# Optimization experiments

Measured on AMD Instinct MI355X. Metric: run time of the kernel, lower is better.

The kernel has to match this reference:

```python
import jax, jax.numpy as jnp
import numpy as np

B, V, S, F, K = 8, 2048, 4, 64, 8
MAX_DIST = np.float32(np.finfo(np.float32).max)


def setup_inputs() -> dict:
    key = jax.random.key(0)
    k1, k2 = jax.random.split(key)
    coordinates = jax.random.normal(k1, (B, V, S), dtype=jnp.float32)
    features = jax.random.normal(k2, (B, V, F), dtype=jnp.float32)
    # per-event number of active vertices (float, compared against the raw mask)
    active_vertices = jnp.full((B, 1), 0.75 * V, dtype=jnp.float32)
    return {"coordinates": coordinates, "features": features,
            "active_vertices": active_vertices}


def reference(coordinates, features, active_vertices):
    # squared euclidean distance matrix: |x_i - x_j|^2 = -2 x_i.x_j + |x_i|^2 + |x_j|^2
    sub = -2.0 * jnp.einsum('bvs,bws->bvw', coordinates, coordinates)
    dot = jnp.sum(coordinates * coordinates, axis=2)  # [B, V]
    dist = jnp.abs(sub + dot[:, :, None] + dot[:, None, :])  # [B, V, V]

    # raw mask: max(row_idx, col_idx); vertex pair valid iff both < n_active
    r = jnp.arange(V)
    raw_mask = jnp.maximum(r[None, :], r[:, None]).astype(jnp.float32)  # [V, V]
    mask = raw_mask[None, :, :] < active_vertices[:, :, None]  # [B, V, V]
    dist = jnp.where(mask, dist, MAX_DIST)

    # top-k smallest distances (self at rank 0 is dropped)
    neg_ranked, idx = jax.lax.top_k(-dist, K)  # [B, V, K]
    neighbour_idx = idx[:, :, 1:]              # [B, V, K-1]
    neighbour_distances = -neg_ranked[:, :, 1:]

    # gather neighbour features per batch: [B, V, K-1, F]
    batch_idx = jnp.arange(B)[:, None, None]
    neighbour_features = features[batch_idx, neighbour_idx]
    return neighbour_distances, neighbour_features
```

## Files before the change

kernel.cpp:

```cpp
#include <hip/hip_runtime.h>
#include <cstdint>
#include <cfloat>
#include <cstddef>

#define BB 8
#define VV 2048
#define SS 4
#define FF 64
#define KK 8

#define BF16_SAFE_MAX 3.3e38f

typedef unsigned long long u64;
typedef unsigned int u32;

static __forceinline__ __device__ double mk_key(float sd_clamped, u32 w) {
    return __longlong_as_double(
        __double_as_longlong((double)sd_clamped) | (long long)w);
}
static __forceinline__ __device__ u32 key_idx(double k) {
    return (u32)((u64)__double_as_longlong(k) & (u64)(VV - 1));
}
static __forceinline__ __device__ double shfl_xor_f64(double x, int m) {
    const u64 b = (u64)__double_as_longlong(x);
    int lo = __shfl_xor((int)(u32)b, m, 64);
    int hi = __shfl_xor((int)(u32)(b >> 32), m, 64);
    return __longlong_as_double((long long)(((u64)(u32)hi << 32) | (u32)lo));
}

#define CED(A, x, y) { double lo_ = fmin(A[x], A[y]);                          \
                       double hi_ = fmax(A[x], A[y]);                          \
                       A[x] = lo_; A[y] = hi_; }

#define SORT8D(K, O)                                                           \
    CED(K,O+0,O+1) CED(K,O+2,O+3) CED(K,O+4,O+5) CED(K,O+6,O+7)                \
    CED(K,O+0,O+2) CED(K,O+1,O+3) CED(K,O+4,O+6) CED(K,O+5,O+7)                \
    CED(K,O+1,O+2) CED(K,O+5,O+6)                                              \
    CED(K,O+0,O+4) CED(K,O+1,O+5) CED(K,O+2,O+6) CED(K,O+3,O+7)                \
    CED(K,O+2,O+4) CED(K,O+3,O+5)                                              \
    CED(K,O+1,O+2) CED(K,O+3,O+4) CED(K,O+5,O+6)

#define CLEAN8D(t)                                                             \
    CED(t,0,4) CED(t,1,5) CED(t,2,6) CED(t,3,7)                                \
    CED(t,0,2) CED(t,1,3) CED(t,4,6) CED(t,5,7)                                \
    CED(t,0,1) CED(t,2,3) CED(t,4,5) CED(t,6,7)

#define MERGE8D(T, S) {                                                        \
    double t[KK];                                                              \
    t[0] = fmin(T[0], S[7]);  t[1] = fmin(T[1], S[6]);                         \
    t[2] = fmin(T[2], S[5]);  t[3] = fmin(T[3], S[4]);                         \
    t[4] = fmin(T[4], S[3]);  t[5] = fmin(T[5], S[2]);                         \
    t[6] = fmin(T[6], S[1]);  t[7] = fmin(T[7], S[0]);                         \
    CLEAN8D(t)                                                                 \
    T[0]=t[0]; T[1]=t[1]; T[2]=t[2]; T[3]=t[3];                                \
    T[4]=t[4]; T[5]=t[5]; T[6]=t[6]; T[7]=t[7]; }

#define BATCH_S8(M, S8)                                                        \
    {                                                                          \
        double bk[16];                                                         \
        _Pragma("unroll")                                                      \
        for (int k = 0; k < 16; ++k) {                                         \
            const int w  = (((M) << 4) + k) * 32 + l;           \
            const int wi = w & (VV / 2 - 1);                  \
            const float4 cw = sc[wi];                                          \
            const float  nw = sn[wi];                                          \
            float q0 = cv.x*cw.x, q1 = cv.y*cw.y,                              \
                  q2 = cv.z*cw.z, q3 = cv.w*cw.w;                              \
            float dotp = ((q0 + q1) + q2) + q3;         \
            float sd = dotp + nvp;                                             \
            sd = sd + nw;                                                      \
            const float sda = fminf(fabsf(sd), FLT_MAX);                       \
            bk[k] = mk_key(sda, (u32)w);                                       \
        }                                                                      \
        SORT8D(bk, 0)                                                          \
        SORT8D(bk, 8)                                                          \
        S8[0] = fmin(bk[0], bk[15]); S8[1] = fmin(bk[1], bk[14]);              \
        S8[2] = fmin(bk[2], bk[13]); S8[3] = fmin(bk[3], bk[12]);              \
        S8[4] = fmin(bk[4], bk[11]); S8[5] = fmin(bk[5], bk[10]);              \
        S8[6] = fmin(bk[6], bk[9]);  S8[7] = fmin(bk[7], bk[8]);               \
        CLEAN8D(S8)                                                            \
    }

__global__ __launch_bounds__(256, 6)
void knn_topk_kernel(const float* __restrict__ coords,
                     const float* __restrict__ feats,
                     const float* __restrict__ active,
                     float* __restrict__ out_dist,
                     float* __restrict__ out_feat)
{
#pragma clang fp contract(off)
    __shared__ float4 sc[VV / 2];
    __shared__ float  sn[VV / 2];

    const int b   = blockIdx.y;
    const int tid = threadIdx.x;
    const int l   = tid & 31;
    const int j   = tid >> 5;
    const int v   = blockIdx.x + (j << 8);

    const float A = active[b];
    int Ai = (int)ceilf(A);
    Ai = Ai < 0 ? 0 : (Ai > VV ? VV : Ai);

    const size_t row = (size_t)b * VV + v;
    const float4* cg = reinterpret_cast<const float4*>(coords + (size_t)b * VV * SS);

    const bool rowActive = ((float)v < A);
    const bool heavy = (__ballot(rowActive) != 0ULL);

    const float4 cv = cg[v];
    float qp0 = cv.x*cv.x, qp1 = cv.y*cv.y, qp2 = cv.z*cv.z, qp3 = cv.w*cv.w;
    const float nv  = ((qp0 + qp1) + qp2) + qp3;
    const float nvp = rowActive ? nv : FLT_MAX;

    double top[KK];

    int ntiles = (Ai + 31) >> 5;
    if (ntiles < 16) ntiles = 16;
    const int nb = (ntiles + 15) >> 4;

#define STAGE(P, LIM)                                                          \
    for (int i = tid; i < (LIM); i += 256) {                                   \
        const float4 c = cg[i + ((P) << 10)];                                  \
        float p0 = c.x*c.x, p1 = c.y*c.y, p2 = c.z*c.z, p3 = c.w*c.w;          \
        const float nrm = ((p0 + p1) + p2) + p3;                               \
        sn[i] = ((i + ((P) << 10)) < Ai) ? nrm : FLT_MAX;                      \
        float4 c2;                                                             \
        c2.x = -2.0f*c.x; c2.y = -2.0f*c.y;                                    \
        c2.z = -2.0f*c.z; c2.w = -2.0f*c.w;                 \
        sc[i] = c2;                                                            \
    }

    STAGE(0, VV / 2)
    __syncthreads();
    if (heavy) {
        BATCH_S8(0, top)
        if (nb > 1) {
            double s8[KK];
            BATCH_S8(1, s8)
            MERGE8D(top, s8)
        }
    }

    if (nb > 2) {
        const int lim2 = (nb << 9) - 1024;
        __syncthreads();
        STAGE(1, lim2)
        __syncthreads();
        if (heavy) {
            {
                double s8[KK];
                BATCH_S8(2, s8)
                MERGE8D(top, s8)
            }
            if (nb > 3) {
                double s8[KK];
                BATCH_S8(3, s8)
                MERGE8D(top, s8)
            }
        }
    }
#undef STAGE

    if (!heavy) {
        if (l >= 1 && l < KK)
            out_dist[row * (KK - 1) + (l - 1)] = BF16_SAFE_MAX;
#pragma unroll
        for (int r = 1; r < KK; ++r) {
            const float2 val = reinterpret_cast<const float2*>(
                feats + ((size_t)b * VV + r) * FF)[l];
            reinterpret_cast<float2*>(out_feat + (row * (KK - 1) + (r - 1)) * FF)[l] = val;
        }
        return;
    }

#pragma unroll
    for (int step = 1; step < 32; step <<= 1) {
        double t[KK];
#pragma unroll
        for (int i = 0; i < KK; ++i) {
            double pb = shfl_xor_f64(top[KK - 1 - i], step);
            t[i] = fmin(top[i], pb);
        }
        CLEAN8D(t)
#pragma unroll
        for (int i = 0; i < KK; ++i) top[i] = t[i];
    }

    float dsel = 0.0f;
#pragma unroll
    for (int r = 1; r < KK; ++r) dsel = (l == r) ? (float)top[r] : dsel;
    if (l >= 1 && l < KK) {
        float d = dsel;
        if (!(d <= BF16_SAFE_MAX)) d = BF16_SAFE_MAX;
        out_dist[row * (KK - 1) + (l - 1)] = d;
    }

#pragma unroll
    for (int r = 1; r < KK; ++r) {
        const u32 idx = key_idx(top[r]);
        const float2 val = reinterpret_cast<const float2*>(
            feats + ((size_t)b * VV + idx) * FF)[l];
        reinterpret_cast<float2*>(out_feat + (row * (KK - 1) + (r - 1)) * FF)[l] = val;
    }
}

extern "C" void kernel_launch(void* const* d_in, const int* in_sizes, int n_in,
                              void* d_out, int out_size, void* d_ws, size_t ws_size,
                              hipStream_t stream)
{
    const float* coords = (const float*)d_in[0];
    const float* feats  = (const float*)d_in[1];
    const float* act    = (const float*)d_in[2];
    float* out_dist = (float*)d_out;
    float* out_feat = out_dist + (size_t)BB * VV * (KK - 1);

    dim3 grid(VV / 8, BB);
    knn_topk_kernel<<<grid, dim3(256), 0, stream>>>(coords, feats, act,
                                                    out_dist, out_feat);
}
```

Baseline: 25.86 us.

## Double rows per block and process candidates in 8-wide batches

```diff
diff --git a/kernel.cpp b/kernel.cpp
--- a/kernel.cpp
+++ b/kernel.cpp
@@ -55,12 +55,11 @@
     T[0]=t[0]; T[1]=t[1]; T[2]=t[2]; T[3]=t[3];                                \
     T[4]=t[4]; T[5]=t[5]; T[6]=t[6]; T[7]=t[7]; }
 
-#define BATCH_S8(M, S8)                                                        \
+#define BATCH_FILL(M, BK)                                                      \
     {                                                                          \
-        double bk[16];                                                         \
         _Pragma("unroll")                                                      \
-        for (int k = 0; k < 16; ++k) {                                         \
-            const int w  = (((M) << 4) + k) * 32 + l;           \
+        for (int k = 0; k < 8; ++k) {                                          \
+            const int w  = (((M) << 3) + k) * 32 + l;           \
             const int wi = w & (VV / 2 - 1);                  \
             const float4 cw = sc[wi];                                          \
             const float  nw = sn[wi];                                          \
@@ -70,18 +69,19 @@
             float sd = dotp + nvp;                                             \
             sd = sd + nw;                                                      \
             const float sda = fminf(fabsf(sd), FLT_MAX);                       \
-            bk[k] = mk_key(sda, (u32)w);                                       \
+            BK[k] = mk_key(sda, (u32)w);                                       \
         }                                                                      \
-        SORT8D(bk, 0)                                                          \
-        SORT8D(bk, 8)                                                          \
-        S8[0] = fmin(bk[0], bk[15]); S8[1] = fmin(bk[1], bk[14]);              \
-        S8[2] = fmin(bk[2], bk[13]); S8[3] = fmin(bk[3], bk[12]);              \
-        S8[4] = fmin(bk[4], bk[11]); S8[5] = fmin(bk[5], bk[10]);              \
-        S8[6] = fmin(bk[6], bk[9]);  S8[7] = fmin(bk[7], bk[8]);               \
-        CLEAN8D(S8)                                                            \
-    }
-
-__global__ __launch_bounds__(256, 6)
+        SORT8D(BK, 0)                                                          \
+    }
+
+#define BATCH_MERGE(M)                                                         \
+    {                                                                          \
+        double bk[KK];                                                         \
+        BATCH_FILL(M, bk)                                                      \
+        MERGE8D(top, bk)                                                       \
+    }
+
+__global__ __launch_bounds__(512, 8)
 void knn_topk_kernel(const float* __restrict__ coords,
                      const float* __restrict__ feats,
                      const float* __restrict__ active,
@@ -96,7 +96,7 @@
     const int tid = threadIdx.x;
     const int l   = tid & 31;
     const int j   = tid >> 5;
-    const int v   = blockIdx.x + (j << 8);
+    const int v   = blockIdx.x + (j << 7);
 
     const float A = active[b];
     int Ai = (int)ceilf(A);
@@ -116,11 +116,11 @@
     double top[KK];
 
     int ntiles = (Ai + 31) >> 5;
-    if (ntiles < 16) ntiles = 16;
-    const int nb = (ntiles + 15) >> 4;
+    if (ntiles < 8) ntiles = 8;
+    const int nb8 = (ntiles + 7) >> 3;
 
 #define STAGE(P, LIM)                                                          \
-    for (int i = tid; i < (LIM); i += 256) {                                   \
+    for (int i = tid; i < (LIM); i += 512) {                                   \
         const float4 c = cg[i + ((P) << 10)];                                  \
         float p0 = c.x*c.x, p1 = c.y*c.y, p2 = c.z*c.z, p3 = c.w*c.w;          \
         const float nrm = ((p0 + p1) + p2) + p3;                               \
@@ -134,30 +134,22 @@
     STAGE(0, VV / 2)
     __syncthreads();
     if (heavy) {
-        BATCH_S8(0, top)
-        if (nb > 1) {
-            double s8[KK];
-            BATCH_S8(1, s8)
-            MERGE8D(top, s8)
-        }
-    }
-
-    if (nb > 2) {
-        const int lim2 = (nb << 9) - 1024;
+        BATCH_FILL(0, top)
+        if (nb8 > 1) BATCH_MERGE(1)
+        if (nb8 > 2) BATCH_MERGE(2)
+        if (nb8 > 3) BATCH_MERGE(3)
+    }
+
+    if (nb8 > 4) {
+        const int lim2 = (nb8 << 8) - 1024;
         __syncthreads();
         STAGE(1, lim2)
         __syncthreads();
         if (heavy) {
-            {
-                double s8[KK];
-                BATCH_S8(2, s8)
-                MERGE8D(top, s8)
-            }
-            if (nb > 3) {
-                double s8[KK];
-                BATCH_S8(3, s8)
-                MERGE8D(top, s8)
-            }
+            BATCH_MERGE(4)
+            if (nb8 > 5) BATCH_MERGE(5)
+            if (nb8 > 6) BATCH_MERGE(6)
+            if (nb8 > 7) BATCH_MERGE(7)
         }
     }
 #undef STAGE
@@ -215,7 +207,7 @@
     float* out_dist = (float*)d_out;
     float* out_feat = out_dist + (size_t)BB * VV * (KK - 1);
 
-    dim3 grid(VV / 8, BB);
-    knn_topk_kernel<<<grid, dim3(256), 0, stream>>>(coords, feats, act,
+    dim3 grid(VV / 16, BB);
+    knn_topk_kernel<<<grid, dim3(512), 0, stream>>>(coords, feats, act,
                                                     out_dist, out_feat);
 }
```

Result: faster. 24.30 us (median of 2 runs) (-6.0%).
